# Optimization experiments

Hardware: AMD Instinct MI355X
Metric: run time of the kernel (lower is better)

## Reference

```python
import jax, jax.numpy as jnp
import numpy as np

B, M, D, DP = 8192, 64, 128, 128

def setup_inputs() -> dict:
    key = jax.random.key(0)
    kx, kq, kk, kv, kr = jax.random.split(key, 5)
    scale = 1.0 / np.sqrt(D)  # keep softmax logits in a sane range
    return {
        "x": jax.random.normal(kx, (B, M, D), dtype=jnp.float32),
        "Wq": jax.random.normal(kq, (D, DP), dtype=jnp.float32) * scale,
        "Wk": jax.random.normal(kk, (D, DP), dtype=jnp.float32) * scale,
        "Wv": jax.random.normal(kv, (D, DP), dtype=jnp.float32) * scale,
        "Wr": jax.random.normal(kr, (D, DP), dtype=jnp.float32) * scale,
    }

def reference(x, Wq, Wk, Wv, Wr):
    # Shared per-field linear projections (Product layer): [B, M, d] @ [d, d'] -> [B, M, d']
    q = jnp.einsum('bmd,de->bme', x, Wq)
    k = jnp.einsum('bmd,de->bme', x, Wk)
    v = jnp.einsum('bmd,de->bme', x, Wv)
    r = jnp.einsum('bmd,de->bme', x, Wr)
    # Field-wise attention: scores [B, M, M], softmax over last axis (axis=2)
    scores = jnp.einsum('bme,bne->bmn', q, k)
    alphas = jax.nn.softmax(scores, axis=2)
    new_e = jnp.einsum('bmn,bne->bme', alphas, v)
    return jax.nn.relu(r + new_e)
```

## Files before the change

### kernel.cpp

```cpp
#include <hip/hip_runtime.h>

typedef _Float16 half8 __attribute__((ext_vector_type(8)));
typedef _Float16 half4 __attribute__((ext_vector_type(4)));
typedef __fp16 fp16x2 __attribute__((ext_vector_type(2)));
typedef float floatx4 __attribute__((ext_vector_type(4)));

#define NB 8
#define SX 136
#define SVT 72

__global__ void wconv_kernel(const float* __restrict__ Wq, const float* __restrict__ Wk,
                             const float* __restrict__ Wv, const float* __restrict__ Wr,
                             _Float16* __restrict__ Wh) {
    int idx = blockIdx.x * 256 + threadIdx.x;
    int row = idx >> 9;
    int col = idx & 511;
    const float* s = (col < 128) ? Wq : (col < 256) ? Wk : (col < 384) ? Wv : Wr;
    Wh[idx] = (_Float16)s[row * 128 + (col & 127)];
}

__global__ __launch_bounds__(512, 2)
void autoint_kernel(const float* __restrict__ xg, const _Float16* __restrict__ Wh,
                    float* __restrict__ outg) {
    const int tid  = threadIdx.x;
    const int w    = tid >> 6;
    const int lane = tid & 63;
    const int nn   = lane & 15;
    const int q    = lane >> 4;
    const int qp   = q & 1, qh = q >> 1;
    const long b0  = (long)blockIdx.x * NB;

    __shared__ _Float16 lds[52736];
    _Float16* Xs0 = lds;
    _Float16* Xs1 = lds + 8704;
    _Float16* Qs  = lds + 17408;
    _Float16* Ks  = lds + 26112;
    _Float16* Rs  = lds + 34816;
    _Float16* Vt  = lds + 43520;

    half8 wf[4][4];
    #pragma unroll
    for (int g = 0; g < 4; ++g) {
        const int col = g * 128 + w * 16 + nn;
        #pragma unroll
        for (int ks = 0; ks < 4; ++ks) {
            half8 f;
            #pragma unroll
            for (int i = 0; i < 8; ++i)
                f[i] = Wh[(ks * 32 + q * 8 + i) * 512 + col];
            wf[g][ks] = f;
        }
    }

    float4 pf[4];
    {
        const float4* Xg = (const float4*)(xg + b0 * 8192);
        #pragma unroll
        for (int t = 0; t < 4; ++t) pf[t] = Xg[t * 512 + tid];
        #pragma unroll
        for (int t = 0; t < 4; ++t) {
            int g = t * 512 + tid;
            int row = g >> 5, c4 = (g & 31) * 4;
            half4 h = { (_Float16)pf[t].x, (_Float16)pf[t].y,
                        (_Float16)pf[t].z, (_Float16)pf[t].w };
            *(half4*)(Xs0 + row * SX + c4) = h;
        }
    }
    __syncthreads();

    #pragma unroll 2
    for (int it = 0; it < NB; ++it) {
        const long b = b0 + it;
        const _Float16* Xc = (it & 1) ? Xs1 : Xs0;
        _Float16*       Xn = (it & 1) ? Xs0 : Xs1;

        if (it + 1 < NB) {
            const float4* Xg = (const float4*)(xg + (b + 1) * 8192);
            #pragma unroll
            for (int t = 0; t < 4; ++t) pf[t] = Xg[t * 512 + tid];
        }

        floatx4 acc[4][4];
        {
            floatx4 z = {0.f, 0.f, 0.f, 0.f};
            #pragma unroll
            for (int rt = 0; rt < 4; ++rt)
                #pragma unroll
                for (int g = 0; g < 4; ++g) acc[rt][g] = z;
        }
        #pragma unroll
        for (int ks = 0; ks < 4; ++ks) {
            half8 a[4];
            #pragma unroll
            for (int rt = 0; rt < 4; ++rt)
                a[rt] = *(const half8*)(Xc + (rt * 16 + nn) * SX + ks * 32 + q * 8);
            #pragma unroll
            for (int rt = 0; rt < 4; ++rt)
                #pragma unroll
                for (int g = 0; g < 4; ++g)
                    acc[rt][g] = __builtin_amdgcn_mfma_f32_16x16x32_f16(
                        a[rt], wf[g][ks], acc[rt][g], 0, 0, 0);
        }

        const int fc = w * 16 + nn;
        #pragma unroll
        for (int rt = 0; rt < 4; ++rt) {
            const int r0 = rt * 16 + q * 4;
            #pragma unroll
            for (int r = 0; r < 4; ++r) Qs[(r0 + r) * SX + fc] = (_Float16)acc[rt][0][r];
            #pragma unroll
            for (int r = 0; r < 4; ++r) Ks[(r0 + r) * SX + fc] = (_Float16)acc[rt][1][r];
            half4 hv = { (_Float16)acc[rt][2][0], (_Float16)acc[rt][2][1],
                         (_Float16)acc[rt][2][2], (_Float16)acc[rt][2][3] };
            *(half4*)(Vt + fc * SVT + r0) = hv;
            #pragma unroll
            for (int r = 0; r < 4; ++r) Rs[(r0 + r) * SX + fc] = (_Float16)acc[rt][3][r];
        }

        if (it + 1 < NB) {
            #pragma unroll
            for (int t = 0; t < 4; ++t) {
                int g = t * 512 + tid;
                int row = g >> 5, c4 = (g & 31) * 4;
                half4 h = { (_Float16)pf[t].x, (_Float16)pf[t].y,
                            (_Float16)pf[t].z, (_Float16)pf[t].w };
                *(half4*)(Xn + row * SX + c4) = h;
            }
        }

        __syncthreads();

        const int mt = w & 3;
        const int eb = (w >> 2) * 4;

        floatx4 sacc[4];
        {
            floatx4 z = {0.f, 0.f, 0.f, 0.f};
            #pragma unroll
            for (int nt = 0; nt < 4; ++nt) sacc[nt] = z;
        }
        #pragma unroll
        for (int ks = 0; ks < 4; ++ks) {
            half8 bq = *(const half8*)(Qs + (mt * 16 + nn) * SX + ks * 32 + q * 8);
            #pragma unroll
            for (int nt = 0; nt < 4; ++nt) {
                half8 ak = *(const half8*)(Ks + (nt * 16 + nn) * SX + ks * 32 + q * 8);
                sacc[nt] = __builtin_amdgcn_mfma_f32_16x16x32_f16(ak, bq, sacc[nt], 0, 0, 0);
            }
        }

        float mx = sacc[0][0];
        #pragma unroll
        for (int nt = 0; nt < 4; ++nt)
            #pragma unroll
            for (int r = 0; r < 4; ++r) mx = fmaxf(mx, sacc[nt][r]);
        mx = fmaxf(mx, __shfl_xor(mx, 16));
        mx = fmaxf(mx, __shfl_xor(mx, 32));
        float ex[4][4];
        float sum = 0.f;
        #pragma unroll
        for (int nt = 0; nt < 4; ++nt)
            #pragma unroll
            for (int r = 0; r < 4; ++r) {
                ex[nt][r] = __expf(sacc[nt][r] - mx);
                sum += ex[nt][r];
            }
        sum += __shfl_xor(sum, 16);
        sum += __shfl_xor(sum, 32);
        const float inv = 1.0f / sum;

        unsigned pku[4][2];
        #pragma unroll
        for (int nt = 0; nt < 4; ++nt)
            #pragma unroll
            for (int h = 0; h < 2; ++h) {
                union { fp16x2 h2; unsigned u; } cv;
                cv.h2 = __builtin_amdgcn_cvt_pkrtz(ex[nt][2 * h] * inv, ex[nt][2 * h + 1] * inv);
                pku[nt][h] = cv.u;
            }

        unsigned af2[2][4];
        #pragma unroll
        for (int c = 0; c < 8; ++c) {
            const int ks2 = (c >> 1) & 1;
            const int h   = c & 1;
            const int lo  = c >> 2;
            unsigned gv = (qp ^ lo) ? pku[2 * ks2 + 1][h] : pku[2 * ks2][h];
            int srcl = ((qp << 1) + (qh ^ lo)) * 16 + nn;
            af2[ks2][h + 2 * lo] = (unsigned)__shfl((int)gv, srcl);
        }
        #pragma unroll
        for (int ks2 = 0; ks2 < 2; ++ks2) {
            unsigned a0 = af2[ks2][0], a1 = af2[ks2][1], a2 = af2[ks2][2], a3 = af2[ks2][3];
            af2[ks2][0] = qh ? a2 : a0;
            af2[ks2][1] = qh ? a3 : a1;
            af2[ks2][2] = qh ? a0 : a2;
            af2[ks2][3] = qh ? a1 : a3;
        }
        half8 af[2];
        #pragma unroll
        for (int ks2 = 0; ks2 < 2; ++ks2) {
            union { unsigned u[4]; half8 h; } uu;
            uu.u[0] = af2[ks2][0]; uu.u[1] = af2[ks2][1];
            uu.u[2] = af2[ks2][2]; uu.u[3] = af2[ks2][3];
            af[ks2] = uu.h;
        }

        floatx4 pv[4];
        {
            floatx4 z = {0.f, 0.f, 0.f, 0.f};
            #pragma unroll
            for (int cc = 0; cc < 4; ++cc) pv[cc] = z;
        }
        #pragma unroll
        for (int ks2 = 0; ks2 < 2; ++ks2)
            #pragma unroll
            for (int cc = 0; cc < 4; ++cc) {
                half8 bv = *(const half8*)(Vt + ((eb + cc) * 16 + nn) * SVT + ks2 * 32 + q * 8);
                pv[cc] = __builtin_amdgcn_mfma_f32_16x16x32_f16(af[ks2], bv, pv[cc], 0, 0, 0);
            }

        float* ob = outg + b * 8192;
        #pragma unroll
        for (int cc = 0; cc < 4; ++cc) {
            const int col = (eb + cc) * 16 + nn;
            #pragma unroll
            for (int r = 0; r < 4; ++r) {
                const int row = mt * 16 + q * 4 + r;
                float rv = (float)Rs[row * SX + col];
                ob[row * 128 + col] = fmaxf(rv + pv[cc][r], 0.0f);
            }
        }

        __syncthreads();
    }
}

extern "C" void kernel_launch(void* const* d_in, const int* in_sizes, int n_in,
                              void* d_out, int out_size, void* d_ws, size_t ws_size,
                              hipStream_t stream) {
    const float* x  = (const float*)d_in[0];
    const float* Wq = (const float*)d_in[1];
    const float* Wk = (const float*)d_in[2];
    const float* Wv = (const float*)d_in[3];
    const float* Wr = (const float*)d_in[4];
    _Float16* Wh = (_Float16*)d_ws;
    float* out = (float*)d_out;

    wconv_kernel<<<256, 256, 0, stream>>>(Wq, Wk, Wv, Wr, Wh);
    autoint_kernel<<<1024, 512, 0, stream>>>(x, Wh, out);
}
```

Baseline: 468.7 us.

## Load x fragments directly from global and drop LDS staging to raise occupancy

Removes the double-buffered LDS staging of x and the register prefetch. Each wave now reads its MFMA A-fragments straight from global memory, converting fp32 to fp16 in registers. LDS use drops from about 103KB to about 69KB per block, and launch bounds are raised to 4 blocks per CU to hide latency through occupancy. The trade-offs are that each x element is read from global by 8 waves instead of once, the explicit overlap of the next-batch load with compute is lost, and registers per thread are squeezed to fit the higher occupancy target.

```diff
diff --git a/kernel.cpp b/kernel.cpp
--- a/kernel.cpp
+++ b/kernel.cpp
@@ -19,7 +19,7 @@
     Wh[idx] = (_Float16)s[row * 128 + (col & 127)];
 }
 
-__global__ __launch_bounds__(512, 2)
+__global__ __launch_bounds__(512, 4)
 void autoint_kernel(const float* __restrict__ xg, const _Float16* __restrict__ Wh,
                     float* __restrict__ outg) {
     const int tid  = threadIdx.x;
@@ -30,13 +30,11 @@
     const int qp   = q & 1, qh = q >> 1;
     const long b0  = (long)blockIdx.x * NB;
 
-    __shared__ _Float16 lds[52736];
-    _Float16* Xs0 = lds;
-    _Float16* Xs1 = lds + 8704;
-    _Float16* Qs  = lds + 17408;
-    _Float16* Ks  = lds + 26112;
-    _Float16* Rs  = lds + 34816;
-    _Float16* Vt  = lds + 43520;
+    __shared__ _Float16 lds[35328];
+    _Float16* Qs = lds;
+    _Float16* Ks = lds + 8704;
+    _Float16* Rs = lds + 17408;
+    _Float16* Vt = lds + 26112;
 
     half8 wf[4][4];
     #pragma unroll
@@ -52,33 +50,9 @@
         }
     }
 
-    float4 pf[4];
-    {
-        const float4* Xg = (const float4*)(xg + b0 * 8192);
-        #pragma unroll
-        for (int t = 0; t < 4; ++t) pf[t] = Xg[t * 512 + tid];
-        #pragma unroll
-        for (int t = 0; t < 4; ++t) {
-            int g = t * 512 + tid;
-            int row = g >> 5, c4 = (g & 31) * 4;
-            half4 h = { (_Float16)pf[t].x, (_Float16)pf[t].y,
-                        (_Float16)pf[t].z, (_Float16)pf[t].w };
-            *(half4*)(Xs0 + row * SX + c4) = h;
-        }
-    }
-    __syncthreads();
-
-    #pragma unroll 2
     for (int it = 0; it < NB; ++it) {
         const long b = b0 + it;
-        const _Float16* Xc = (it & 1) ? Xs1 : Xs0;
-        _Float16*       Xn = (it & 1) ? Xs0 : Xs1;
-
-        if (it + 1 < NB) {
-            const float4* Xg = (const float4*)(xg + (b + 1) * 8192);
-            #pragma unroll
-            for (int t = 0; t < 4; ++t) pf[t] = Xg[t * 512 + tid];
-        }
+        const float* Xb = xg + b * 8192;
 
         floatx4 acc[4][4];
         {
@@ -92,8 +66,14 @@
         for (int ks = 0; ks < 4; ++ks) {
             half8 a[4];
             #pragma unroll
-            for (int rt = 0; rt < 4; ++rt)
-                a[rt] = *(const half8*)(Xc + (rt * 16 + nn) * SX + ks * 32 + q * 8);
+            for (int rt = 0; rt < 4; ++rt) {
+                const float* p = Xb + (rt * 16 + nn) * 128 + ks * 32 + q * 8;
+                float4 f0 = *(const float4*)(p);
+                float4 f1 = *(const float4*)(p + 4);
+                half8 h = { (_Float16)f0.x, (_Float16)f0.y, (_Float16)f0.z, (_Float16)f0.w,
+                            (_Float16)f1.x, (_Float16)f1.y, (_Float16)f1.z, (_Float16)f1.w };
+                a[rt] = h;
+            }
             #pragma unroll
             for (int rt = 0; rt < 4; ++rt)
                 #pragma unroll
@@ -115,17 +95,6 @@
             *(half4*)(Vt + fc * SVT + r0) = hv;
             #pragma unroll
             for (int r = 0; r < 4; ++r) Rs[(r0 + r) * SX + fc] = (_Float16)acc[rt][3][r];
-        }
-
-        if (it + 1 < NB) {
-            #pragma unroll
-            for (int t = 0; t < 4; ++t) {
-                int g = t * 512 + tid;
-                int row = g >> 5, c4 = (g & 31) * 4;
-                half4 h = { (_Float16)pf[t].x, (_Float16)pf[t].y,
-                            (_Float16)pf[t].z, (_Float16)pf[t].w };
-                *(half4*)(Xn + row * SX + c4) = h;
-            }
         }
 
         __syncthreads();
```

Result: slower. 874.0 us (+86.5%).

## Software-pipeline projection of next batch under attention, swizzle Q/K LDS, defer softmax normalization

Applied to the files above, without the earlier changes.

Restructures the per-batch loop so the projection MFMAs for batch it+1 are issued right after the score MFMAs of batch it. The global load for batch it+2 is issued at the same point, so projection work can overlap softmax and PV. Q/K LDS writes and reads gain an XOR swizzle to cut bank conflicts. R is stored transposed so the epilogue reads it as half4. Softmax normalization moves from the probabilities to the PV output via a per-row shuffle of the inverse sum. The cost is more live registers (acc stays alive across the attention phase), which may hurt occupancy at 512 threads with 2 blocks per CU, plus slightly more LDS.

```diff
diff --git a/kernel.cpp b/kernel.cpp
--- a/kernel.cpp
+++ b/kernel.cpp
@@ -30,13 +30,13 @@
     const int qp   = q & 1, qh = q >> 1;
     const long b0  = (long)blockIdx.x * NB;
 
-    __shared__ _Float16 lds[52736];
+    __shared__ _Float16 lds[53248];
     _Float16* Xs0 = lds;
     _Float16* Xs1 = lds + 8704;
     _Float16* Qs  = lds + 17408;
     _Float16* Ks  = lds + 26112;
-    _Float16* Rs  = lds + 34816;
-    _Float16* Vt  = lds + 43520;
+    _Float16* Rt  = lds + 34816;
+    _Float16* Vt  = lds + 44032;
 
     half8 wf[4][4];
     #pragma unroll
@@ -53,41 +53,29 @@
     }
 
     float4 pf[4];
-    {
-        const float4* Xg = (const float4*)(xg + b0 * 8192);
+    floatx4 acc[4][4];
+
+    auto load_x = [&](long b) {
+        const float4* Xg = (const float4*)(xg + b * 8192);
         #pragma unroll
         for (int t = 0; t < 4; ++t) pf[t] = Xg[t * 512 + tid];
+    };
+    auto write_xs = [&](_Float16* Xd) {
         #pragma unroll
         for (int t = 0; t < 4; ++t) {
             int g = t * 512 + tid;
             int row = g >> 5, c4 = (g & 31) * 4;
             half4 h = { (_Float16)pf[t].x, (_Float16)pf[t].y,
                         (_Float16)pf[t].z, (_Float16)pf[t].w };
-            *(half4*)(Xs0 + row * SX + c4) = h;
-        }
-    }
-    __syncthreads();
-
-    #pragma unroll 2
-    for (int it = 0; it < NB; ++it) {
-        const long b = b0 + it;
-        const _Float16* Xc = (it & 1) ? Xs1 : Xs0;
-        _Float16*       Xn = (it & 1) ? Xs0 : Xs1;
-
-        if (it + 1 < NB) {
-            const float4* Xg = (const float4*)(xg + (b + 1) * 8192);
-            #pragma unroll
-            for (int t = 0; t < 4; ++t) pf[t] = Xg[t * 512 + tid];
-        }
-
-        floatx4 acc[4][4];
-        {
-            floatx4 z = {0.f, 0.f, 0.f, 0.f};
-            #pragma unroll
-            for (int rt = 0; rt < 4; ++rt)
-                #pragma unroll
-                for (int g = 0; g < 4; ++g) acc[rt][g] = z;
-        }
+            *(half4*)(Xd + row * SX + c4) = h;
+        }
+    };
+    auto proj = [&](const _Float16* Xc) {
+        floatx4 z = {0.f, 0.f, 0.f, 0.f};
+        #pragma unroll
+        for (int rt = 0; rt < 4; ++rt)
+            #pragma unroll
+            for (int g = 0; g < 4; ++g) acc[rt][g] = z;
         #pragma unroll
         for (int ks = 0; ks < 4; ++ks) {
             half8 a[4];
@@ -101,37 +89,42 @@
                     acc[rt][g] = __builtin_amdgcn_mfma_f32_16x16x32_f16(
                         a[rt], wf[g][ks], acc[rt][g], 0, 0, 0);
         }
-
-        const int fc = w * 16 + nn;
+    };
+    auto scatter = [&]() {
+        const int fc  = w * 16 + nn;
+        const int fcq = fc ^ (qh << 4);
         #pragma unroll
         for (int rt = 0; rt < 4; ++rt) {
             const int r0 = rt * 16 + q * 4;
             #pragma unroll
-            for (int r = 0; r < 4; ++r) Qs[(r0 + r) * SX + fc] = (_Float16)acc[rt][0][r];
-            #pragma unroll
-            for (int r = 0; r < 4; ++r) Ks[(r0 + r) * SX + fc] = (_Float16)acc[rt][1][r];
+            for (int r = 0; r < 4; ++r) Qs[(r0 + r) * SX + fcq] = (_Float16)acc[rt][0][r];
+            #pragma unroll
+            for (int r = 0; r < 4; ++r) Ks[(r0 + r) * SX + fcq] = (_Float16)acc[rt][1][r];
             half4 hv = { (_Float16)acc[rt][2][0], (_Float16)acc[rt][2][1],
                          (_Float16)acc[rt][2][2], (_Float16)acc[rt][2][3] };
             *(half4*)(Vt + fc * SVT + r0) = hv;
-            #pragma unroll
-            for (int r = 0; r < 4; ++r) Rs[(r0 + r) * SX + fc] = (_Float16)acc[rt][3][r];
-        }
-
-        if (it + 1 < NB) {
-            #pragma unroll
-            for (int t = 0; t < 4; ++t) {
-                int g = t * 512 + tid;
-                int row = g >> 5, c4 = (g & 31) * 4;
-                half4 h = { (_Float16)pf[t].x, (_Float16)pf[t].y,
-                            (_Float16)pf[t].z, (_Float16)pf[t].w };
-                *(half4*)(Xn + row * SX + c4) = h;
-            }
-        }
-
-        __syncthreads();
-
-        const int mt = w & 3;
-        const int eb = (w >> 2) * 4;
+            half4 hr = { (_Float16)acc[rt][3][0], (_Float16)acc[rt][3][1],
+                         (_Float16)acc[rt][3][2], (_Float16)acc[rt][3][3] };
+            *(half4*)(Rt + fc * SVT + r0) = hr;
+        }
+    };
+
+    load_x(b0);
+    write_xs(Xs0);
+    __syncthreads();
+    load_x(b0 + 1);
+    proj(Xs0);
+    scatter();
+    write_xs(Xs1);
+    __syncthreads();
+
+    const int mt = w & 3;
+    const int eb = (w >> 2) * 4;
+    const int swz = (nn >> 3) << 4;
+
+    #pragma unroll 2
+    for (int it = 0; it < NB; ++it) {
+        const long b = b0 + it;
 
         floatx4 sacc[4];
         {
@@ -141,13 +134,16 @@
         }
         #pragma unroll
         for (int ks = 0; ks < 4; ++ks) {
-            half8 bq = *(const half8*)(Qs + (mt * 16 + nn) * SX + ks * 32 + q * 8);
+            half8 bq = *(const half8*)(Qs + (mt * 16 + nn) * SX + ((ks * 32 + q * 8) ^ swz));
             #pragma unroll
             for (int nt = 0; nt < 4; ++nt) {
-                half8 ak = *(const half8*)(Ks + (nt * 16 + nn) * SX + ks * 32 + q * 8);
+                half8 ak = *(const half8*)(Ks + (nt * 16 + nn) * SX + ((ks * 32 + q * 8) ^ swz));
                 sacc[nt] = __builtin_amdgcn_mfma_f32_16x16x32_f16(ak, bq, sacc[nt], 0, 0, 0);
             }
         }
+
+        if (it + 2 < NB) load_x(b + 2);
+        if (it + 1 < NB) proj((it & 1) ? Xs0 : Xs1);
 
         float mx = sacc[0][0];
         #pragma unroll
@@ -175,7 +171,7 @@
             #pragma unroll
             for (int h = 0; h < 2; ++h) {
                 union { fp16x2 h2; unsigned u; } cv;
-                cv.h2 = __builtin_amdgcn_cvt_pkrtz(ex[nt][2 * h] * inv, ex[nt][2 * h + 1] * inv);
+                cv.h2 = __builtin_amdgcn_cvt_pkrtz(ex[nt][2 * h], ex[nt][2 * h + 1]);
                 pku[nt][h] = cv.u;
             }
 
@@ -220,19 +216,28 @@
                 pv[cc] = __builtin_amdgcn_mfma_f32_16x16x32_f16(af[ks2], bv, pv[cc], 0, 0, 0);
             }
 
+        float invr[4];
+        #pragma unroll
+        for (int r = 0; r < 4; ++r) invr[r] = __shfl(inv, q * 4 + r);
         float* ob = outg + b * 8192;
         #pragma unroll
         for (int cc = 0; cc < 4; ++cc) {
             const int col = (eb + cc) * 16 + nn;
+            half4 rv4 = *(const half4*)(Rt + col * SVT + mt * 16 + q * 4);
             #pragma unroll
             for (int r = 0; r < 4; ++r) {
                 const int row = mt * 16 + q * 4 + r;
-                float rv = (float)Rs[row * SX + col];
-                ob[row * 128 + col] = fmaxf(rv + pv[cc][r], 0.0f);
+                ob[row * 128 + col] = fmaxf((float)rv4[r] + pv[cc][r] * invr[r], 0.0f);
             }
         }
 
         __syncthreads();
+
+        if (it + 1 < NB) {
+            scatter();
+            if (it + 2 < NB) write_xs((it & 1) ? Xs1 : Xs0);
+            __syncthreads();
+        }
     }
 }
 
```

New measurement: 491.6 us. 1.05x slower.
